# Performance work log

Hardware: AMD Instinct MI355X
Metric: run time of the kernel (lower is better)

## Reference

```python
import jax, jax.numpy as jnp
import numpy as np

N = 20000
E = 320000
F_IN = 50
HID = 64          # hidden_channels
HEADS = 8
WIDTH = HID * HEADS  # 512
NUM_CLASSES = 121


def setup_inputs() -> dict:
    key = jax.random.key(0)
    ks = jax.random.split(key, 16)
    def p(k, shape, fan_in):
        return (jax.random.normal(k, shape, dtype=jnp.float32) / np.sqrt(fan_in)).astype(jnp.float32)
    x = jax.random.normal(ks[0], (N, F_IN), dtype=jnp.float32)
    edge_index = jax.random.randint(ks[1], (2, E), 0, N, dtype=jnp.int64)
    return {
        "x": x,
        "edge_index": edge_index,
        # layer 1: 50 -> 64, heads=8, concat
        "W1": p(ks[2], (F_IN, HEADS * HID), F_IN),
        "a1_src": p(ks[3], (HEADS, HID), HID),
        "a1_dst": p(ks[4], (HEADS, HID), HID),
        "b1": jnp.zeros((HEADS * HID,), jnp.float32),
        # layer 2: 512 -> 512, heads=1, concat
        "W2": p(ks[5], (WIDTH, WIDTH), WIDTH),
        "a2_src": p(ks[6], (1, WIDTH), WIDTH),
        "a2_dst": p(ks[7], (1, WIDTH), WIDTH),
        "b2": jnp.zeros((WIDTH,), jnp.float32),
        # layer 3: 512 -> 121, heads=1, concat=False (mean)
        "W3": p(ks[8], (WIDTH, NUM_CLASSES), WIDTH),
        "a3_src": p(ks[9], (1, NUM_CLASSES), NUM_CLASSES),
        "a3_dst": p(ks[10], (1, NUM_CLASSES), NUM_CLASSES),
        "b3": jnp.zeros((NUM_CLASSES,), jnp.float32),
    }


def gat_conv(x, src, dst, W, a_src, a_dst, b, heads, out_ch, concat):
    n = x.shape[0]
    h = (x @ W).reshape(n, heads, out_ch)                 # [N, H, C]
    al_s = jnp.sum(h * a_src, axis=-1)                     # [N, H]
    al_d = jnp.sum(h * a_dst, axis=-1)                     # [N, H]
    e = jax.nn.leaky_relu(al_s[src] + al_d[dst], 0.2)      # [E, H]
    # edge softmax per destination node (stable)
    m = jax.ops.segment_max(e, dst, num_segments=n)        # [N, H]
    m = jnp.where(jnp.isfinite(m), m, 0.0)
    ex = jnp.exp(e - m[dst])
    z = jax.ops.segment_sum(ex, dst, num_segments=n)       # [N, H]
    alpha = ex / (z[dst] + 1e-16)                          # [E, H]
    msg = h[src] * alpha[..., None]                        # [E, H, C]
    out = jax.ops.segment_sum(msg, dst, num_segments=n)    # [N, H, C]
    out = out.reshape(n, heads * out_ch) if concat else out.mean(axis=1)
    return out + b


def reference(x, edge_index, W1, a1_src, a1_dst, b1, W2, a2_src, a2_dst, b2, W3, a3_src, a3_dst, b3):
    n = x.shape[0]
    # PyG GATConv adds self loops by default
    loops = jnp.arange(n, dtype=edge_index.dtype)
    src = jnp.concatenate([edge_index[0], loops])
    dst = jnp.concatenate([edge_index[1], loops])
    # eval mode: dropout is identity
    x1 = gat_conv(x, src, dst, W1, a1_src, a1_dst, b1, HEADS, HID, True)
    h = jax.nn.elu(x1)
    x1 = gat_conv(h, src, dst, W2, a2_src, a2_dst, b2, 1, WIDTH, True)
    h = jax.nn.elu(x1)
    x1 = gat_conv(h, src, dst, W3, a3_src, a3_dst, b3, 1, NUM_CLASSES, False)
    return x1
```

## Files before the change

### kernel.cpp

```cpp
#include <hip/hip_runtime.h>
#include <hip/hip_bf16.h>
#include <hip/hip_fp16.h>

#define NN     20000
#define ERAW   320000
#define ETOT   (ERAW + NN)
#define F_IN   50
#define HID    64
#define HEADS  8
#define WIDTH  512
#define NCLS   121
#define NCLS_P 128

typedef __attribute__((ext_vector_type(8))) __bf16 bf16x8;
typedef __attribute__((ext_vector_type(4))) float floatx4;

__device__ __forceinline__ unsigned short f32_to_bf16_rn(float f) {
  unsigned u = __float_as_uint(f);
  unsigned r = u + 0x7fffu + ((u >> 16) & 1u);
  return (unsigned short)(r >> 16);
}
__device__ __forceinline__ void split_one(float f, unsigned short& h,
                                          unsigned short& l) {
  h = f32_to_bf16_rn(f);
  float fh = __uint_as_float(((unsigned)h) << 16);
  l = f32_to_bf16_rn(f - fh);
}

__device__ __forceinline__ float2 u2f2(unsigned u) {
  __half2 hv = *reinterpret_cast<__half2*>(&u);
  return __half22float2(hv);
}

__device__ __forceinline__ void gll16(const unsigned short* g,
                                      const unsigned short* l) {
  __builtin_amdgcn_global_load_lds(
      (const __attribute__((address_space(1))) unsigned int*)(const void*)g,
      (__attribute__((address_space(3))) unsigned int*)(void*)l, 16, 0, 0);
}

#define PW_BLOCKS 449
__global__ __launch_bounds__(256) void prep_weights(
    const float* __restrict__ W1, const float* __restrict__ W2,
    const float* __restrict__ W3, const float* __restrict__ a1s,
    const float* __restrict__ a1d, unsigned short* __restrict__ w1hHi,
    unsigned short* __restrict__ w1hLo, unsigned short* __restrict__ w2tHi,
    unsigned short* __restrict__ w2tLo, unsigned short* __restrict__ w3tHi,
    unsigned short* __restrict__ w3tLo, float* __restrict__ w1as,
    float* __restrict__ w1ad) {
  __shared__ float t[32][33];
  const int b = blockIdx.x;
  if (b < 320) {
    const float* W;
    unsigned short *thi, *tlo;
    int M, Mp, bx, by;
    const int K = WIDTH;
    if (b < 256) {
      W = W2; thi = w2tHi; tlo = w2tLo; M = WIDTH; Mp = WIDTH;
      bx = b & 15; by = b >> 4;
    } else {
      int bb = b - 256;
      W = W3; thi = w3tHi; tlo = w3tLo; M = NCLS; Mp = NCLS_P;
      bx = bb & 15; by = bb >> 4;
    }
    int k0 = bx * 32, m0 = by * 32;
    int tx = threadIdx.x & 31, ty = threadIdx.x >> 5;
    #pragma unroll
    for (int r = 0; r < 4; ++r) {
      int k = k0 + ty + r * 8, m = m0 + tx;
      float v = 0.f;
      if (k < K && m < M) v = W[(size_t)k * M + m];
      t[ty + r * 8][tx] = v;
    }
    __syncthreads();
    #pragma unroll
    for (int r = 0; r < 4; ++r) {
      int m = m0 + ty + r * 8, k = k0 + tx;
      if (m < Mp && k < K) {
        unsigned short h, l;
        split_one(t[tx][ty + r * 8], h, l);
        thi[(size_t)m * K + k] = h;
        tlo[(size_t)m * K + k] = l;
      }
    }
  } else if (b < 448) {
    int idx = (b - 320) * 256 + threadIdx.x;
    if (idx < HEADS * HID * HID) {
      int hd = idx >> 12, rem = idx & 4095;
      int col = rem >> 6, k = rem & 63;
      float v = (k < F_IN) ? W1[(size_t)k * WIDTH + hd * HID + col] : 0.f;
      unsigned short h, l;
      split_one(v, h, l);
      w1hHi[idx] = h;
      w1hLo[idx] = l;
    }
  } else {
    for (int idx = threadIdx.x; idx < 2 * F_IN * HEADS; idx += 256) {
      int which = idx >= F_IN * HEADS;
      int r = which ? idx - F_IN * HEADS : idx;
      int k = r >> 3, h = r & 7;
      const float* a = which ? a1d : a1s;
      float s = 0.f;
      for (int c = 0; c < HID; ++c)
        s += W1[(size_t)k * WIDTH + h * HID + c] * a[h * HID + c];
      (which ? w1ad : w1as)[r] = s;
    }
  }
}

__global__ __launch_bounds__(512) void gemm_split_db(
    const unsigned short* __restrict__ Ahi, const unsigned short* __restrict__ Alo,
    const unsigned short* __restrict__ Bthi, const unsigned short* __restrict__ Btlo,
    __half* __restrict__ C16, int N, int K, int M, int Mp, int RB, int CB) {
  __shared__ unsigned short lds[65536];

  const int f = blockIdx.x;
  const int xcd = f & 7;
  const int g = f >> 3;
  const int cb = g % CB;
  const int rb = (g / CB) * 8 + xcd;
  if (rb >= RB) return;
  const int r0 = rb * 128, c0 = cb * 128;

  const int tid = threadIdx.x;
  const int wave = tid >> 6, lane = tid & 63;
  const int wr = wave >> 2, wc = wave & 3;
  const int lkg = lane >> 4, lmn = lane & 15;

  const int row8 = lane >> 3, cslot = lane & 7;
  const unsigned short* gsrc[8];
  int ldsoff[8];
  #pragma unroll
  for (int i = 0; i < 8; ++i) {
    int q = wave * 8 + i;
    int a = q >> 4, rg = q & 15;
    int r = rg * 8 + row8;
    int c = cslot ^ (r & 7);
    const unsigned short* base =
        (a == 0) ? Ahi : (a == 1) ? Alo : (a == 2) ? Bthi : Btlo;
    size_t grow;
    if (a < 2) {
      int ra = r0 + r;
      if (ra > N - 1) ra = N - 1;
      grow = (size_t)ra;
    } else {
      grow = (size_t)(c0 + r);
    }
    gsrc[i] = base + grow * K + c * 8;
    ldsoff[i] = a * 8192 + rg * 512;
  }

  int rowA[4], m7A[4], rowB[2], m7B[2];
  #pragma unroll
  for (int mi = 0; mi < 4; ++mi) {
    int m = wr * 64 + mi * 16 + lmn;
    rowA[mi] = m * 64;  m7A[mi] = m & 7;
  }
  #pragma unroll
  for (int ni = 0; ni < 2; ++ni) {
    int n = wc * 32 + ni * 16 + lmn;
    rowB[ni] = 16384 + n * 64;  m7B[ni] = n & 7;
  }

  floatx4 acc[4][2] = {};

  #pragma unroll
  for (int i = 0; i < 8; ++i) gll16(gsrc[i], lds + ldsoff[i]);

  const int nk = K >> 6;
  for (int t = 0; t < nk; ++t) {
    if (t + 1 < nk) {
      const unsigned short* dst = lds + ((t + 1) & 1) * 32768;
      #pragma unroll
      for (int i = 0; i < 8; ++i)
        gll16(gsrc[i] + (t + 1) * 64, dst + ldsoff[i]);
      asm volatile("s_waitcnt vmcnt(8)" ::: "memory");
    } else {
      asm volatile("s_waitcnt vmcnt(0)" ::: "memory");
    }
    __builtin_amdgcn_sched_barrier(0);
    __builtin_amdgcn_s_barrier();
    __builtin_amdgcn_sched_barrier(0);

    const unsigned short* Lb = lds + (t & 1) * 32768;
    #pragma unroll
    for (int ksub = 0; ksub < 2; ++ksub) {
      bf16x8 fAhi[4], fAlo[4], fBhi[2], fBlo[2];
      #pragma unroll
      for (int mi = 0; mi < 4; ++mi) {
        int s = rowA[mi] + (((ksub << 2) | lkg) ^ m7A[mi]) * 8;
        fAhi[mi] = *(const bf16x8*)(Lb + s);
        fAlo[mi] = *(const bf16x8*)(Lb + s + 8192);
      }
      #pragma unroll
      for (int ni = 0; ni < 2; ++ni) {
        int s = rowB[ni] + (((ksub << 2) | lkg) ^ m7B[ni]) * 8;
        fBhi[ni] = *(const bf16x8*)(Lb + s);
        fBlo[ni] = *(const bf16x8*)(Lb + s + 8192);
      }
      #pragma unroll
      for (int mi = 0; mi < 4; ++mi)
        #pragma unroll
        for (int ni = 0; ni < 2; ++ni) {
          acc[mi][ni] = __builtin_amdgcn_mfma_f32_16x16x32_bf16(
              fAhi[mi], fBhi[ni], acc[mi][ni], 0, 0, 0);
          acc[mi][ni] = __builtin_amdgcn_mfma_f32_16x16x32_bf16(
              fAhi[mi], fBlo[ni], acc[mi][ni], 0, 0, 0);
          acc[mi][ni] = __builtin_amdgcn_mfma_f32_16x16x32_bf16(
              fAlo[mi], fBhi[ni], acc[mi][ni], 0, 0, 0);
        }
    }

    __builtin_amdgcn_sched_barrier(0);
    asm volatile("s_waitcnt lgkmcnt(0)" ::: "memory");
    __builtin_amdgcn_s_barrier();
    __builtin_amdgcn_sched_barrier(0);
  }

  #pragma unroll
  for (int mi = 0; mi < 4; ++mi) {
    #pragma unroll
    for (int r = 0; r < 4; ++r) {
      int grow = r0 + wr * 64 + mi * 16 + (lane >> 4) * 4 + r;
      if (grow >= N) continue;
      #pragma unroll
      for (int ni = 0; ni < 2; ++ni) {
        int gcol = c0 + wc * 32 + ni * 16 + lmn;
        float v = (gcol < M) ? acc[mi][ni][r] : 0.f;
        C16[(size_t)grow * Mp + gcol] = __float2half(v);
      }
    }
  }
}

__global__ __launch_bounds__(256) void gemm_l1_heads(
    const unsigned short* __restrict__ Ahi, const unsigned short* __restrict__ Alo,
    const unsigned short* __restrict__ Bthi, const unsigned short* __restrict__ Btlo,
    unsigned short* __restrict__ outHi, unsigned short* __restrict__ outLo,
    const float* __restrict__ bias) {
  __shared__ unsigned short sAhi[8192], sAlo[8192], sBhi[4096], sBlo[4096];
  const int tid = threadIdx.x;
  const int wave = tid >> 6, lane = tid & 63;
  const int r0 = blockIdx.x * 128;
  const int hd = blockIdx.y;
  const int lkg = lane >> 4, lmn = lane & 15;

  #pragma unroll
  for (int t = 0; t < 4; ++t) {
    int cid = tid + t * 256;
    int row = cid >> 3, c = cid & 7;
    int gr = r0 + row; if (gr > NN - 1) gr = NN - 1;
    const size_t goff = (size_t)gr * WIDTH + hd * HID + c * 8;
    int loff = (((c >> 2) * 4 + (c & 3)) * 128 + row) * 8;
    *(uint4*)(sAhi + loff) = *(const uint4*)(Ahi + goff);
    *(uint4*)(sAlo + loff) = *(const uint4*)(Alo + goff);
  }
  #pragma unroll
  for (int t = 0; t < 2; ++t) {
    int cid = tid + t * 256;
    int col = cid >> 3, c = cid & 7;
    const size_t goff = (size_t)(hd * HID + col) * HID + c * 8;
    int loff = (((c >> 2) * 4 + (c & 3)) * 64 + col) * 8;
    *(uint4*)(sBhi + loff) = *(const uint4*)(Bthi + goff);
    *(uint4*)(sBlo + loff) = *(const uint4*)(Btlo + goff);
  }
  __syncthreads();

  floatx4 acc[2][4] = {};
  #pragma unroll
  for (int ks = 0; ks < 2; ++ks) {
    bf16x8 fAhi[2], fAlo[2], fBhi[4], fBlo[4];
    #pragma unroll
    for (int mi = 0; mi < 2; ++mi) {
      int m = wave * 32 + mi * 16 + lmn;
      int off = ((ks * 4 + lkg) * 128 + m) * 8;
      fAhi[mi] = *(const bf16x8*)(sAhi + off);
      fAlo[mi] = *(const bf16x8*)(sAlo + off);
    }
    #pragma unroll
    for (int ni = 0; ni < 4; ++ni) {
      int n = ni * 16 + lmn;
      int off = ((ks * 4 + lkg) * 64 + n) * 8;
      fBhi[ni] = *(const bf16x8*)(sBhi + off);
      fBlo[ni] = *(const bf16x8*)(sBlo + off);
    }
    #pragma unroll
    for (int mi = 0; mi < 2; ++mi)
      #pragma unroll
      for (int ni = 0; ni < 4; ++ni) {
        acc[mi][ni] = __builtin_amdgcn_mfma_f32_16x16x32_bf16(
            fAhi[mi], fBhi[ni], acc[mi][ni], 0, 0, 0);
        acc[mi][ni] = __builtin_amdgcn_mfma_f32_16x16x32_bf16(
            fAhi[mi], fBlo[ni], acc[mi][ni], 0, 0, 0);
        acc[mi][ni] = __builtin_amdgcn_mfma_f32_16x16x32_bf16(
            fAlo[mi], fBhi[ni], acc[mi][ni], 0, 0, 0);
      }
  }

  #pragma unroll
  for (int mi = 0; mi < 2; ++mi) {
    #pragma unroll
    for (int r = 0; r < 4; ++r) {
      int grow = r0 + wave * 32 + mi * 16 + (lane >> 4) * 4 + r;
      if (grow >= NN) continue;
      #pragma unroll
      for (int ni = 0; ni < 4; ++ni) {
        int gcol = hd * HID + ni * 16 + lmn;
        float v = acc[mi][ni][r] + bias[gcol];
        v = (v > 0.f) ? v : (__expf(v) - 1.0f);
        unsigned short hh, ll;
        split_one(v, hh, ll);
        outHi[(size_t)grow * WIDTH + gcol] = hh;
        outLo[(size_t)grow * WIDTH + gcol] = ll;
      }
    }
  }
}

__global__ __launch_bounds__(256) void al1_kernel(
    const float* __restrict__ x, const float* __restrict__ w1as,
    const float* __restrict__ w1ad, float* __restrict__ al_s,
    float* __restrict__ al_d) {
  int n = (blockIdx.x * blockDim.x + threadIdx.x) >> 6;
  int lane = threadIdx.x & 63;
  if (n >= NN) return;
  float xv = (lane < F_IN) ? x[(size_t)n * F_IN + lane] : 0.f;
  float ws[HEADS], wd[HEADS];
  #pragma unroll
  for (int h = 0; h < HEADS; ++h) {
    ws[h] = (lane < F_IN) ? w1as[lane * HEADS + h] : 0.f;
    wd[h] = (lane < F_IN) ? w1ad[lane * HEADS + h] : 0.f;
  }
  #pragma unroll
  for (int h = 0; h < HEADS; ++h) {
    float ss = xv * ws[h], sd = xv * wd[h];
    #pragma unroll
    for (int o = 32; o; o >>= 1) {
      ss += __shfl_xor(ss, o);
      sd += __shfl_xor(sd, o);
    }
    if (lane == 0) {
      al_s[n * HEADS + h] = ss;
      al_d[n * HEADS + h] = sd;
    }
  }
}

template <int C, int CS>
__global__ __launch_bounds__(256) void compute_al16(
    const __half* __restrict__ h16, const float* __restrict__ a_src,
    const float* __restrict__ a_dst, float* __restrict__ al_s,
    float* __restrict__ al_d) {
  int n = (blockIdx.x * blockDim.x + threadIdx.x) >> 6;
  int lane = threadIdx.x & 63;
  if (n >= NN) return;
  const __half* hr = h16 + (size_t)n * CS;
  float ss = 0.f, sd = 0.f;
  if (C % 512 == 0) {
    uint4 raw = *(const uint4*)(hr + lane * 8);
    float f[8];
    float2 t;
    t = u2f2(raw.x); f[0] = t.x; f[1] = t.y;
    t = u2f2(raw.y); f[2] = t.x; f[3] = t.y;
    t = u2f2(raw.z); f[4] = t.x; f[5] = t.y;
    t = u2f2(raw.w); f[6] = t.x; f[7] = t.y;
    #pragma unroll
    for (int j = 0; j < 8; ++j) {
      int c = lane * 8 + j;
      ss += f[j] * a_src[c];
      sd += f[j] * a_dst[c];
    }
  } else {
    for (int c = lane; c < C; c += 64) {
      float v = __half2float(hr[c]);
      ss += v * a_src[c];
      sd += v * a_dst[c];
    }
  }
  #pragma unroll
  for (int o = 32; o; o >>= 1) {
    ss += __shfl_xor(ss, o);
    sd += __shfl_xor(sd, o);
  }
  if (lane == 0) {
    al_s[n] = ss;
    al_d[n] = sd;
  }
}

__global__ __launch_bounds__(256) void count_deg(
    const int* __restrict__ edst, int* __restrict__ deg) {
  int e = blockIdx.x * blockDim.x + threadIdx.x;
  if (e >= ETOT) return;
  int d = (e < ERAW) ? edst[e] : (e - ERAW);
  atomicAdd(&deg[d], 1);
}

__global__ __launch_bounds__(256) void scan_deg(
    const int* __restrict__ deg, int* __restrict__ rowptr) {
  __shared__ int part[256];
  const int t = threadIdx.x;
  const int CHUNK = (NN + 255) / 256;
  int lo = t * CHUNK, hi = min(lo + CHUNK, NN);
  int s = 0;
  for (int i = lo; i < hi; ++i) s += deg[i];
  part[t] = s;
  __syncthreads();
  for (int off = 1; off < 256; off <<= 1) {
    int v = (t >= off) ? part[t - off] : 0;
    __syncthreads();
    part[t] += v;
    __syncthreads();
  }
  int base = (t == 0) ? 0 : part[t - 1];
  for (int i = lo; i < hi; ++i) {
    rowptr[i] = base;
    base += deg[i];
  }
  if (t == 255) rowptr[NN] = part[255];
}

__global__ __launch_bounds__(256) void scatter_csr(
    const int* __restrict__ esrc, const int* __restrict__ edst,
    const int* __restrict__ rowptr, int* __restrict__ cnt,
    int* __restrict__ csrc) {
  int e = blockIdx.x * blockDim.x + threadIdx.x;
  if (e >= ETOT) return;
  int s, d;
  if (e < ERAW) { s = esrc[e]; d = edst[e]; }
  else          { s = e - ERAW; d = e - ERAW; }
  int pos = rowptr[d] + atomicAdd(&cnt[d], 1);
  csrc[pos] = s;
}

__global__ __launch_bounds__(256) void agg_x_sm(
    const int* __restrict__ rowptr, const int* __restrict__ csrc,
    const float* __restrict__ al_s, const float* __restrict__ al_d,
    const float* __restrict__ x, unsigned short* __restrict__ outHi,
    unsigned short* __restrict__ outLo) {
  const int w = threadIdx.x >> 6, lane = threadIdx.x & 63;
  const int d = blockIdx.x * 4 + w;
  if (d >= NN) return;
  const int r0 = rowptr[d], r1 = rowptr[d + 1];
  const int mh = lane & 7;
  const float ald_my = al_d[d * HEADS + mh];
  float m_my = al_s[d * HEADS + mh] + ald_my;
  m_my = (m_my > 0.f) ? m_my : 0.2f * m_my;

  float z_my = 0.f;
  float acc[HEADS];
  #pragma unroll
  for (int hh = 0; hh < HEADS; ++hh) acc[hh] = 0.f;

  int p = r0;
  for (; p + 8 <= r1; p += 8) {
    int s[8];
    #pragma unroll
    for (int j = 0; j < 8; ++j) s[j] = csrc[p + j];
    float xv[8];
    #pragma unroll
    for (int j = 0; j < 8; ++j)
      xv[j] = (lane < F_IN) ? x[(size_t)s[j] * F_IN + lane] : 0.f;
    float av[8];
    #pragma unroll
    for (int j = 0; j < 8; ++j) av[j] = al_s[s[j] * HEADS + mh];
    #pragma unroll
    for (int j = 0; j < 8; ++j) {
      float v = av[j] + ald_my;
      v = (v > 0.f) ? v : 0.2f * v;
      float a = __expf(v - m_my);
      z_my += a;
      #pragma unroll
      for (int hh = 0; hh < HEADS; ++hh) acc[hh] += __shfl(a, hh, 8) * xv[j];
    }
  }
  for (; p < r1; ++p) {
    int s = csrc[p];
    float v = al_s[s * HEADS + mh] + ald_my;
    v = (v > 0.f) ? v : 0.2f * v;
    float a = __expf(v - m_my);
    z_my += a;
    float xv = (lane < F_IN) ? x[(size_t)s * F_IN + lane] : 0.f;
    #pragma unroll
    for (int hh = 0; hh < HEADS; ++hh) acc[hh] += __shfl(a, hh, 8) * xv;
  }

  #pragma unroll
  for (int hh = 0; hh < HEADS; ++hh) {
    float zh = __shfl(z_my, hh, 8);
    float v = (lane < F_IN) ? acc[hh] / (zh + 1e-16f) : 0.f;
    unsigned short h2, l2;
    split_one(v, h2, l2);
    outHi[(size_t)d * WIDTH + hh * HID + lane] = h2;
    outLo[(size_t)d * WIDTH + hh * HID + lane] = l2;
  }
}

template <int M, int MS, bool ELU, bool SPLIT>
__global__ __launch_bounds__(256) void pull_agg_sm(
    const int* __restrict__ rowptr, const int* __restrict__ csrc,
    const float* __restrict__ al_s, const float* __restrict__ al_d,
    const __half* __restrict__ h16, const float* __restrict__ bias,
    float* __restrict__ out, unsigned short* __restrict__ outHi,
    unsigned short* __restrict__ outLo) {
  constexpr int EPL = MS / 64;
  const int w = threadIdx.x >> 6;
  const int lane = threadIdx.x & 63;
  const int d = blockIdx.x * 4 + w;
  if (d >= NN) return;
  const int r0 = rowptr[d], r1 = rowptr[d + 1];
  const float ald = al_d[d];
  float m = al_s[d] + ald;
  m = (m > 0.f) ? m : 0.2f * m;

  const int base = lane * EPL;
  const __half* hb = h16 + base;
  float acc[EPL];
  #pragma unroll
  for (int j = 0; j < EPL; ++j) acc[j] = 0.f;
  float z = 0.f;

  int p = r0;
  for (; p + 8 <= r1; p += 8) {
    int s[8];
    #pragma unroll
    for (int j = 0; j < 8; ++j) s[j] = csrc[p + j];
    uint4 raw8[8];
    unsigned raw2[8];
    #pragma unroll
    for (int j = 0; j < 8; ++j) {
      const __half* hr = hb + (size_t)s[j] * MS;
      if (EPL == 8)      raw8[j] = *(const uint4*)hr;
      else if (EPL == 2) raw2[j] = *(const unsigned*)hr;
    }
    float av[8];
    #pragma unroll
    for (int j = 0; j < 8; ++j) av[j] = al_s[s[j]];
    #pragma unroll
    for (int j = 0; j < 8; ++j) {
      float v = av[j] + ald;
      v = (v > 0.f) ? v : 0.2f * v;
      float a = __expf(v - m);
      z += a;
      if (EPL == 8) {
        float2 f0 = u2f2(raw8[j].x), f1 = u2f2(raw8[j].y);
        float2 f2 = u2f2(raw8[j].z), f3 = u2f2(raw8[j].w);
        acc[0] += f0.x * a; acc[1] += f0.y * a;
        acc[2] += f1.x * a; acc[3] += f1.y * a;
        acc[4] += f2.x * a; acc[5] += f2.y * a;
        acc[6] += f3.x * a; acc[7] += f3.y * a;
      } else if (EPL == 2) {
        float2 f0 = u2f2(raw2[j]);
        acc[0] += f0.x * a;
        acc[1] += f0.y * a;
      }
    }
  }
  for (; p < r1; ++p) {
    int s = csrc[p];
    float v = al_s[s] + ald;
    v = (v > 0.f) ? v : 0.2f * v;
    float a = __expf(v - m);
    z += a;
    const __half* hr = hb + (size_t)s * MS;
    if (EPL == 8) {
      uint4 raw = *(const uint4*)hr;
      float2 f0 = u2f2(raw.x), f1 = u2f2(raw.y);
      float2 f2 = u2f2(raw.z), f3 = u2f2(raw.w);
      acc[0] += f0.x * a; acc[1] += f0.y * a;
      acc[2] += f1.x * a; acc[3] += f1.y * a;
      acc[4] += f2.x * a; acc[5] += f2.y * a;
      acc[6] += f3.x * a; acc[7] += f3.y * a;
    } else if (EPL == 2) {
      unsigned raw = *(const unsigned*)hr;
      float2 f0 = u2f2(raw);
      acc[0] += f0.x * a;
      acc[1] += f0.y * a;
    }
  }
  const float iz = 1.0f / (z + 1e-16f);

  #pragma unroll
  for (int j = 0; j < EPL; ++j) {
    if ((M == MS) || (base + j < M)) {
      float v = acc[j] * iz + bias[base + j];
      if (ELU) v = (v > 0.f) ? v : (__expf(v) - 1.0f);
      if (SPLIT) {
        unsigned short hh, ll;
        split_one(v, hh, ll);
        outHi[(size_t)d * M + base + j] = hh;
        outLo[(size_t)d * M + base + j] = ll;
      } else {
        out[(size_t)d * M + base + j] = v;
      }
    }
  }
}

extern "C" void kernel_launch(void* const* d_in, const int* in_sizes, int n_in,
                              void* d_out, int out_size, void* d_ws,
                              size_t ws_size, hipStream_t stream) {
  const float* x      = (const float*)d_in[0];
  const int*   ei     = (const int*)d_in[1];
  const float* W1     = (const float*)d_in[2];
  const float* a1_src = (const float*)d_in[3];
  const float* a1_dst = (const float*)d_in[4];
  const float* b1     = (const float*)d_in[5];
  const float* W2     = (const float*)d_in[6];
  const float* a2_src = (const float*)d_in[7];
  const float* a2_dst = (const float*)d_in[8];
  const float* b2     = (const float*)d_in[9];
  const float* W3     = (const float*)d_in[10];
  const float* a3_src = (const float*)d_in[11];
  const float* a3_dst = (const float*)d_in[12];
  const float* b3     = (const float*)d_in[13];
  float* out = (float*)d_out;

  const int* esrc = ei;
  const int* edst = ei + ERAW;

  unsigned short* p1Hi  = (unsigned short*)d_ws;
  unsigned short* p1Lo  = p1Hi + (size_t)NN * WIDTH;
  unsigned short* p2Hi  = p1Lo + (size_t)NN * WIDTH;
  unsigned short* p2Lo  = p2Hi + (size_t)NN * WIDTH;
  __half*        h16    = (__half*)(p2Lo + (size_t)NN * WIDTH);
  unsigned short* w1hHi = (unsigned short*)(h16 + (size_t)NN * WIDTH);
  unsigned short* w1hLo = w1hHi + (size_t)HEADS * HID * HID;
  unsigned short* w2tHi = w1hLo + (size_t)HEADS * HID * HID;
  unsigned short* w2tLo = w2tHi + (size_t)WIDTH * WIDTH;
  unsigned short* w3tHi = w2tLo + (size_t)WIDTH * WIDTH;
  unsigned short* w3tLo = w3tHi + (size_t)NCLS_P * WIDTH;
  float* al_s   = (float*)(w3tLo + (size_t)NCLS_P * WIDTH);
  float* al_d   = al_s + (size_t)NN * HEADS;
  float* w1as   = al_d + (size_t)NN * HEADS;
  float* w1ad   = w1as + F_IN * HEADS;
  int* deg      = (int*)(w1ad + F_IN * HEADS);
  int* cnt      = deg + NN;
  int* rowptr   = cnt + NN;
  int* csrc     = rowptr + NN + 4;

  hipMemsetAsync(deg, 0, (size_t)(2 * NN) * sizeof(int), stream);
  const int eblk = (ETOT + 255) / 256;
  count_deg<<<eblk, 256, 0, stream>>>(edst, deg);
  scan_deg<<<1, 256, 0, stream>>>(deg, rowptr);
  scatter_csr<<<eblk, 256, 0, stream>>>(esrc, edst, rowptr, cnt, csrc);

  prep_weights<<<PW_BLOCKS, 256, 0, stream>>>(
      W1, W2, W3, a1_src, a1_dst, w1hHi, w1hLo, w2tHi, w2tLo, w3tHi, w3tLo,
      w1as, w1ad);

  const int nwblk = (NN + 3) / 4;

  al1_kernel<<<nwblk, 256, 0, stream>>>(x, w1as, w1ad, al_s, al_d);
  agg_x_sm<<<nwblk, 256, 0, stream>>>(rowptr, csrc, al_s, al_d, x, p1Hi,
                                      p1Lo);
  gemm_l1_heads<<<dim3((NN + 127) / 128, HEADS), 256, 0, stream>>>(
      p1Hi, p1Lo, w1hHi, w1hLo, p2Hi, p2Lo, b1);

  const int RB = (NN + 127) / 128;
  const int RBG = (RB + 7) / 8;

  gemm_split_db<<<RBG * 8 * (WIDTH / 128), 512, 0, stream>>>(
      p2Hi, p2Lo, w2tHi, w2tLo, h16, NN, WIDTH, WIDTH, WIDTH, RB, WIDTH / 128);
  compute_al16<WIDTH, WIDTH><<<nwblk, 256, 0, stream>>>(h16, a2_src, a2_dst,
                                                        al_s, al_d);
  pull_agg_sm<WIDTH, WIDTH, true, true><<<nwblk, 256, 0, stream>>>(
      rowptr, csrc, al_s, al_d, h16, b2, nullptr, p1Hi, p1Lo);

  gemm_split_db<<<RBG * 8 * (NCLS_P / 128), 512, 0, stream>>>(
      p1Hi, p1Lo, w3tHi, w3tLo, h16, NN, WIDTH, NCLS, NCLS_P, RB,
      NCLS_P / 128);
  compute_al16<NCLS, NCLS_P><<<nwblk, 256, 0, stream>>>(h16, a3_src, a3_dst,
                                                        al_s, al_d);
  pull_agg_sm<NCLS, NCLS_P, false, false><<<nwblk, 256, 0, stream>>>(
      rowptr, csrc, al_s, al_d, h16, b3, out, nullptr, nullptr);
}
```

Before: 395.0 us.

## Fuse attention-logit dot products into GEMM epilogue and use smaller tiles for layer 3

Drops the separate compute_al16 kernels. The GEMM epilogue now computes the per-node a_src/a_dst dot products on the fp16-rounded outputs, reduces them across lanes and adds them into zeroed al_s/al_d buffers with atomics. The GEMM is templated on the row-tile size, so layer 3 (128 padded columns) runs with 64-row tiles to get more blocks, and s_setprio is raised around the MFMA bursts. It also widens the degree scan to 1024 threads. In exchange it adds atomics and memsets, and summation order becomes nondeterministic.

Measured after the change: 429.3 us. +8.7%, slower.

```diff
diff --git a/kernel.cpp b/kernel.cpp
--- a/kernel.cpp
+++ b/kernel.cpp
@@ -108,11 +108,18 @@
   }
 }
 
+template <int MI>
 __global__ __launch_bounds__(512) void gemm_split_db(
     const unsigned short* __restrict__ Ahi, const unsigned short* __restrict__ Alo,
     const unsigned short* __restrict__ Bthi, const unsigned short* __restrict__ Btlo,
-    __half* __restrict__ C16, int N, int K, int M, int Mp, int RB, int CB) {
-  __shared__ unsigned short lds[65536];
+    __half* __restrict__ C16, const float* __restrict__ a_src,
+    const float* __restrict__ a_dst, float* __restrict__ al_s,
+    float* __restrict__ al_d, int N, int K, int M, int Mp, int RB, int CB) {
+  constexpr int ABUF = MI * 2048;
+  constexpr int BHALF = MI * 4096;
+  constexpr int BUF = MI * 4096 + 16384;
+  constexpr int NGW = (MI * 8 + 32) / 8;
+  __shared__ unsigned short lds[2 * BUF];
 
   const int f = blockIdx.x;
   const int xcd = f & 7;
@@ -120,7 +127,7 @@
   const int cb = g % CB;
   const int rb = (g / CB) * 8 + xcd;
   if (rb >= RB) return;
-  const int r0 = rb * 128, c0 = cb * 128;
+  const int r0 = rb * (MI * 32), c0 = cb * 128;
 
   const int tid = threadIdx.x;
   const int wave = tid >> 6, lane = tid & 63;
@@ -128,12 +135,15 @@
   const int lkg = lane >> 4, lmn = lane & 15;
 
   const int row8 = lane >> 3, cslot = lane & 7;
-  const unsigned short* gsrc[8];
-  int ldsoff[8];
-  #pragma unroll
-  for (int i = 0; i < 8; ++i) {
-    int q = wave * 8 + i;
-    int a = q >> 4, rg = q & 15;
+  const unsigned short* gsrc[NGW];
+  int ldsoff[NGW];
+  #pragma unroll
+  for (int i = 0; i < NGW; ++i) {
+    int q = wave * NGW + i;
+    int a, rg;
+    if (q < MI * 4)      { a = 0; rg = q; }
+    else if (q < MI * 8) { a = 1; rg = q - MI * 4; }
+    else { int qb = q - MI * 8; a = 2 + (qb >> 4); rg = qb & 15; }
     int r = rg * 8 + row8;
     int c = cslot ^ (r & 7);
     const unsigned short* base =
@@ -147,34 +157,40 @@
       grow = (size_t)(c0 + r);
     }
     gsrc[i] = base + grow * K + c * 8;
-    ldsoff[i] = a * 8192 + rg * 512;
-  }
-
-  int rowA[4], m7A[4], rowB[2], m7B[2];
-  #pragma unroll
-  for (int mi = 0; mi < 4; ++mi) {
-    int m = wr * 64 + mi * 16 + lmn;
+    int aoff = (a == 0) ? 0 : (a == 1) ? ABUF : (a == 2) ? BHALF
+                                              : (BHALF + 8192);
+    ldsoff[i] = aoff + rg * 512;
+  }
+
+  int rowA[MI], m7A[MI], rowB[2], m7B[2];
+  #pragma unroll
+  for (int mi = 0; mi < MI; ++mi) {
+    int m = wr * (MI * 16) + mi * 16 + lmn;
     rowA[mi] = m * 64;  m7A[mi] = m & 7;
   }
   #pragma unroll
   for (int ni = 0; ni < 2; ++ni) {
     int n = wc * 32 + ni * 16 + lmn;
-    rowB[ni] = 16384 + n * 64;  m7B[ni] = n & 7;
-  }
-
-  floatx4 acc[4][2] = {};
-
-  #pragma unroll
-  for (int i = 0; i < 8; ++i) gll16(gsrc[i], lds + ldsoff[i]);
+    rowB[ni] = BHALF + n * 64;  m7B[ni] = n & 7;
+  }
+
+  floatx4 acc[MI][2] = {};
+
+  #pragma unroll
+  for (int i = 0; i < NGW; ++i) gll16(gsrc[i], lds + ldsoff[i]);
 
   const int nk = K >> 6;
   for (int t = 0; t < nk; ++t) {
     if (t + 1 < nk) {
-      const unsigned short* dst = lds + ((t + 1) & 1) * 32768;
-      #pragma unroll
-      for (int i = 0; i < 8; ++i)
+      const unsigned short* dst = lds + ((t + 1) & 1) * BUF;
+      #pragma unroll
+      for (int i = 0; i < NGW; ++i)
         gll16(gsrc[i] + (t + 1) * 64, dst + ldsoff[i]);
-      asm volatile("s_waitcnt vmcnt(8)" ::: "memory");
+      if constexpr (MI == 4) {
+        asm volatile("s_waitcnt vmcnt(8)" ::: "memory");
+      } else {
+        asm volatile("s_waitcnt vmcnt(6)" ::: "memory");
+      }
     } else {
       asm volatile("s_waitcnt vmcnt(0)" ::: "memory");
     }
@@ -182,15 +198,15 @@
     __builtin_amdgcn_s_barrier();
     __builtin_amdgcn_sched_barrier(0);
 
-    const unsigned short* Lb = lds + (t & 1) * 32768;
+    const unsigned short* Lb = lds + (t & 1) * BUF;
     #pragma unroll
     for (int ksub = 0; ksub < 2; ++ksub) {
-      bf16x8 fAhi[4], fAlo[4], fBhi[2], fBlo[2];
-      #pragma unroll
-      for (int mi = 0; mi < 4; ++mi) {
+      bf16x8 fAhi[MI], fAlo[MI], fBhi[2], fBlo[2];
+      #pragma unroll
+      for (int mi = 0; mi < MI; ++mi) {
         int s = rowA[mi] + (((ksub << 2) | lkg) ^ m7A[mi]) * 8;
         fAhi[mi] = *(const bf16x8*)(Lb + s);
-        fAlo[mi] = *(const bf16x8*)(Lb + s + 8192);
+        fAlo[mi] = *(const bf16x8*)(Lb + s + ABUF);
       }
       #pragma unroll
       for (int ni = 0; ni < 2; ++ni) {
@@ -198,8 +214,9 @@
         fBhi[ni] = *(const bf16x8*)(Lb + s);
         fBlo[ni] = *(const bf16x8*)(Lb + s + 8192);
       }
-      #pragma unroll
-      for (int mi = 0; mi < 4; ++mi)
+      __builtin_amdgcn_s_setprio(1);
+      #pragma unroll
+      for (int mi = 0; mi < MI; ++mi)
         #pragma unroll
         for (int ni = 0; ni < 2; ++ni) {
           acc[mi][ni] = __builtin_amdgcn_mfma_f32_16x16x32_bf16(
@@ -209,6 +226,7 @@
           acc[mi][ni] = __builtin_amdgcn_mfma_f32_16x16x32_bf16(
               fAlo[mi], fBhi[ni], acc[mi][ni], 0, 0, 0);
         }
+      __builtin_amdgcn_s_setprio(0);
     }
 
     __builtin_amdgcn_sched_barrier(0);
@@ -218,16 +236,31 @@
   }
 
   #pragma unroll
-  for (int mi = 0; mi < 4; ++mi) {
+  for (int mi = 0; mi < MI; ++mi) {
     #pragma unroll
     for (int r = 0; r < 4; ++r) {
-      int grow = r0 + wr * 64 + mi * 16 + (lane >> 4) * 4 + r;
-      if (grow >= N) continue;
+      int grow = r0 + wr * (MI * 16) + mi * 16 + lkg * 4 + r;
+      float psum = 0.f, dsum = 0.f;
       #pragma unroll
       for (int ni = 0; ni < 2; ++ni) {
         int gcol = c0 + wc * 32 + ni * 16 + lmn;
         float v = (gcol < M) ? acc[mi][ni][r] : 0.f;
-        C16[(size_t)grow * Mp + gcol] = __float2half(v);
+        __half hv = __float2half(v);
+        if (grow < N) C16[(size_t)grow * Mp + gcol] = hv;
+        float vr = __half2float(hv);
+        float as = (gcol < M) ? a_src[gcol] : 0.f;
+        float ad = (gcol < M) ? a_dst[gcol] : 0.f;
+        psum += vr * as;
+        dsum += vr * ad;
+      }
+      #pragma unroll
+      for (int o = 1; o < 16; o <<= 1) {
+        psum += __shfl_xor(psum, o);
+        dsum += __shfl_xor(dsum, o);
+      }
+      if (lmn == 0 && grow < N) {
+        atomicAdd(&al_s[grow], psum);
+        atomicAdd(&al_d[grow], dsum);
       }
     }
   }
@@ -346,48 +379,6 @@
   }
 }
 
-template <int C, int CS>
-__global__ __launch_bounds__(256) void compute_al16(
-    const __half* __restrict__ h16, const float* __restrict__ a_src,
-    const float* __restrict__ a_dst, float* __restrict__ al_s,
-    float* __restrict__ al_d) {
-  int n = (blockIdx.x * blockDim.x + threadIdx.x) >> 6;
-  int lane = threadIdx.x & 63;
-  if (n >= NN) return;
-  const __half* hr = h16 + (size_t)n * CS;
-  float ss = 0.f, sd = 0.f;
-  if (C % 512 == 0) {
-    uint4 raw = *(const uint4*)(hr + lane * 8);
-    float f[8];
-    float2 t;
-    t = u2f2(raw.x); f[0] = t.x; f[1] = t.y;
-    t = u2f2(raw.y); f[2] = t.x; f[3] = t.y;
-    t = u2f2(raw.z); f[4] = t.x; f[5] = t.y;
-    t = u2f2(raw.w); f[6] = t.x; f[7] = t.y;
-    #pragma unroll
-    for (int j = 0; j < 8; ++j) {
-      int c = lane * 8 + j;
-      ss += f[j] * a_src[c];
-      sd += f[j] * a_dst[c];
-    }
-  } else {
-    for (int c = lane; c < C; c += 64) {
-      float v = __half2float(hr[c]);
-      ss += v * a_src[c];
-      sd += v * a_dst[c];
-    }
-  }
-  #pragma unroll
-  for (int o = 32; o; o >>= 1) {
-    ss += __shfl_xor(ss, o);
-    sd += __shfl_xor(sd, o);
-  }
-  if (lane == 0) {
-    al_s[n] = ss;
-    al_d[n] = sd;
-  }
-}
-
 __global__ __launch_bounds__(256) void count_deg(
     const int* __restrict__ edst, int* __restrict__ deg) {
   int e = blockIdx.x * blockDim.x + threadIdx.x;
@@ -396,17 +387,17 @@
   atomicAdd(&deg[d], 1);
 }
 
-__global__ __launch_bounds__(256) void scan_deg(
+__global__ __launch_bounds__(1024) void scan_deg(
     const int* __restrict__ deg, int* __restrict__ rowptr) {
-  __shared__ int part[256];
+  __shared__ int part[1024];
   const int t = threadIdx.x;
-  const int CHUNK = (NN + 255) / 256;
+  const int CHUNK = (NN + 1023) / 1024;
   int lo = t * CHUNK, hi = min(lo + CHUNK, NN);
   int s = 0;
   for (int i = lo; i < hi; ++i) s += deg[i];
   part[t] = s;
   __syncthreads();
-  for (int off = 1; off < 256; off <<= 1) {
+  for (int off = 1; off < 1024; off <<= 1) {
     int v = (t >= off) ? part[t - off] : 0;
     __syncthreads();
     part[t] += v;
@@ -417,7 +408,7 @@
     rowptr[i] = base;
     base += deg[i];
   }
-  if (t == 255) rowptr[NN] = part[255];
+  if (t == 1023) rowptr[NN] = part[1023];
 }
 
 __global__ __launch_bounds__(256) void scatter_csr(
@@ -642,7 +633,7 @@
   hipMemsetAsync(deg, 0, (size_t)(2 * NN) * sizeof(int), stream);
   const int eblk = (ETOT + 255) / 256;
   count_deg<<<eblk, 256, 0, stream>>>(edst, deg);
-  scan_deg<<<1, 256, 0, stream>>>(deg, rowptr);
+  scan_deg<<<1, 1024, 0, stream>>>(deg, rowptr);
   scatter_csr<<<eblk, 256, 0, stream>>>(esrc, edst, rowptr, cnt, csrc);
 
   prep_weights<<<PW_BLOCKS, 256, 0, stream>>>(
@@ -657,21 +648,23 @@
   gemm_l1_heads<<<dim3((NN + 127) / 128, HEADS), 256, 0, stream>>>(
       p1Hi, p1Lo, w1hHi, w1hLo, p2Hi, p2Lo, b1);
 
-  const int RB = (NN + 127) / 128;
-  const int RBG = (RB + 7) / 8;
-
-  gemm_split_db<<<RBG * 8 * (WIDTH / 128), 512, 0, stream>>>(
-      p2Hi, p2Lo, w2tHi, w2tLo, h16, NN, WIDTH, WIDTH, WIDTH, RB, WIDTH / 128);
-  compute_al16<WIDTH, WIDTH><<<nwblk, 256, 0, stream>>>(h16, a2_src, a2_dst,
-                                                        al_s, al_d);
+  const int RB2 = (NN + 127) / 128;
+  const int G2 = ((RB2 + 7) / 8) * 8 * (WIDTH / 128);
+  hipMemsetAsync(al_s, 0, (size_t)NN * sizeof(float), stream);
+  hipMemsetAsync(al_d, 0, (size_t)NN * sizeof(float), stream);
+  gemm_split_db<4><<<G2, 512, 0, stream>>>(
+      p2Hi, p2Lo, w2tHi, w2tLo, h16, a2_src, a2_dst, al_s, al_d, NN, WIDTH,
+      WIDTH, WIDTH, RB2, WIDTH / 128);
   pull_agg_sm<WIDTH, WIDTH, true, true><<<nwblk, 256, 0, stream>>>(
       rowptr, csrc, al_s, al_d, h16, b2, nullptr, p1Hi, p1Lo);
 
-  gemm_split_db<<<RBG * 8 * (NCLS_P / 128), 512, 0, stream>>>(
-      p1Hi, p1Lo, w3tHi, w3tLo, h16, NN, WIDTH, NCLS, NCLS_P, RB,
-      NCLS_P / 128);
-  compute_al16<NCLS, NCLS_P><<<nwblk, 256, 0, stream>>>(h16, a3_src, a3_dst,
-                                                        al_s, al_d);
+  const int RB3 = (NN + 63) / 64;
+  const int G3 = ((RB3 + 7) / 8) * 8 * (NCLS_P / 128);
+  hipMemsetAsync(al_s, 0, (size_t)NN * sizeof(float), stream);
+  hipMemsetAsync(al_d, 0, (size_t)NN * sizeof(float), stream);
+  gemm_split_db<2><<<G3, 512, 0, stream>>>(
+      p1Hi, p1Lo, w3tHi, w3tLo, h16, a3_src, a3_dst, al_s, al_d, NN, WIDTH,
+      NCLS, NCLS_P, RB3, NCLS_P / 128);
   pull_agg_sm<NCLS, NCLS_P, false, false><<<nwblk, 256, 0, stream>>>(
       rowptr, csrc, al_s, al_d, h16, b3, out, nullptr, nullptr);
 }
```
